# Kernel optimization log

Hardware: AMD Instinct MI355X
Metric: run time of the kernel (lower is better)

Reference implementation:

```python
import jax, jax.numpy as jnp
import numpy as np
from jax import lax

WIN = 7  # hard-coded winsize in PSF.forward
EPS = 1e-8


def _box_sum(x, n):
    # Sliding n x n window sum with zero padding (== ZeroPad2d(n//2) + unfold sum),
    return lax.reduce_window(x, 0.0, lax.add, (1, 1, n, n), (1, 1, 1, 1), 'SAME')


def _patch_stats(x, n):
    n2 = n * n
    s = _box_sum(x, n)
    s2 = _box_sum(x * x, n)
    mean = s / n2
    # torch .var() default is unbiased (divide by N-1)
    var = (s2 - n2 * mean * mean) / (n2 - 1)
    return mean, jnp.maximum(var, 0.0)


def patch_mv_norm(x, n):
    mean, var = _patch_stats(x, n)
    return (x - mean) / (jnp.sqrt(var) + EPS)


def patch_adain(x, y, n):
    x_norm = patch_mv_norm(x, n)
    y_mean, y_var = _patch_stats(y, n)
    return x_norm * jnp.sqrt(y_var) + y_mean  # note: no eps on y_std, as in source


def conv1x1(x, w, b):
    # x: (B,C,H,W), w: (O,C), b: (O,)
    return jnp.einsum('oc,bchw->bohw', w, x) + b[None, :, None, None]


def setup_inputs() -> dict:
    key = jax.random.key(0)
    ks = jax.random.split(key, 12)
    B, C, H, W = 8, 256, 128, 128
    front = jax.random.normal(ks[0], (B, C, H, W), dtype=jnp.float32)
    back = jax.random.normal(ks[1], (B, C, H, W), dtype=jnp.float32)
    mask = jax.random.uniform(ks[2], (B, 1, H, W), dtype=jnp.float32)
    scale = 0.02
    we = jax.random.normal(ks[3], (C, C), dtype=jnp.float32) * scale
    wf = jax.random.normal(ks[4], (C, C), dtype=jnp.float32) * scale
    wg = jax.random.normal(ks[5], (C, C), dtype=jnp.float32) * scale
    wh = jax.random.normal(ks[6], (C, C), dtype=jnp.float32) * scale
    be = jax.random.normal(ks[7], (C,), dtype=jnp.float32) * scale
    bf = jax.random.normal(ks[8], (C,), dtype=jnp.float32) * scale
    bg = jax.random.normal(ks[9], (C,), dtype=jnp.float32) * scale
    bh = jax.random.normal(ks[10], (C,), dtype=jnp.float32) * scale
    return {'front': front, 'back': back, 'mask': mask,
            'we': we, 'be': be, 'wf': wf, 'bf': bf,
            'wg': wg, 'bg': bg, 'wh': wh, 'bh': bh}


def reference(front, back, mask, we, be, wf, bf, wg, bg, wh, bh):
    b, c, h, w = front.shape
    EE = conv1x1(patch_adain(front, back, WIN), we, be)
    FF = conv1x1(patch_mv_norm(front, WIN), wf, bf)
    GG = conv1x1(patch_mv_norm(back, WIN), wg, bg)
    HH = conv1x1(back, wh, bh)
    # channel-wise cosine similarity between FF and GG
    F_n = jnp.sqrt(jnp.sum(FF * FF, axis=1))  # (B,H,W)
    G_n = jnp.sqrt(jnp.sum(GG * GG, axis=1))
    S = jnp.sum(FF * GG, axis=1) / (F_n * G_n)
    # per-sample spatial min-max normalization
    S_flat = S.reshape(b, h * w)
    s_min = jnp.min(S_flat, axis=1, keepdims=True)
    s_max = jnp.max(S_flat, axis=1, keepdims=True)
    S_n = ((S_flat - s_min) / (s_max - s_min)).reshape(b, 1, h, w)
    fused = S_n * EE + (1.0 - S_n) * HH
    return fused
```

## Files before the change

### kernel.cpp

```cpp
#include <hip/hip_runtime.h>
#include <math.h>

#define PIX 16384
#define TSZ ((size_t)33554432)

typedef __attribute__((ext_vector_type(8))) short  short8;
typedef __attribute__((ext_vector_type(4))) float  float4v;
typedef __attribute__((ext_vector_type(4))) unsigned int uint4v;
typedef __attribute__((ext_vector_type(2))) unsigned int uint2v;

__device__ __forceinline__ unsigned short f2bf(float x) {
  unsigned int u = __float_as_uint(x);
  u += 0x7fffu + ((u >> 16) & 1u);
  return (unsigned short)(u >> 16);
}
__device__ __forceinline__ float bf2f(unsigned short h) {
  return __uint_as_float(((unsigned int)h) << 16);
}
__device__ __forceinline__ unsigned int pack_bf2(float lo, float hi) {
  unsigned int ul = __float_as_uint(lo); ul += 0x7fffu + ((ul >> 16) & 1u);
  unsigned int uh = __float_as_uint(hi); uh += 0x7fffu + ((uh >> 16) & 1u);
  return __builtin_amdgcn_perm(uh, ul, 0x07060302u);
}

#define SB0   __builtin_amdgcn_sched_barrier(0)
#define BARR  __builtin_amdgcn_s_barrier()
#define LGKM0 asm volatile("s_waitcnt lgkmcnt(0)" ::: "memory")
#define VMC(n) asm volatile("s_waitcnt vmcnt(" #n ")" ::: "memory")

__global__ __launch_bounds__(256) void k_prep(const float* __restrict__ we,
                                              const float* __restrict__ wf,
                                              const float* __restrict__ wg,
                                              const float* __restrict__ wh,
                                              unsigned short* __restrict__ wbf) {
  int idx = blockIdx.x * 256 + threadIdx.x;
  int g = idx >> 16, within = idx & 65535;
  const float* src = (g == 0) ? wf : (g == 1) ? wg : (g == 2) ? we : wh;
  int e    = within & 7;
  int lane = (within >> 3) & 63;
  int im   = (within >> 9) & 3;
  int wv   = (within >> 11) & 3;
  int i    = within >> 13;
  int col = lane & 15, q = lane >> 4;
  int m = wv * 64 + im * 16 + col;
  int k = i * 32 + q * 8 + e;
  wbf[idx] = f2bf(src[m * 256 + k]);
}

__global__ __launch_bounds__(256, 4) void k_stats(const float* __restrict__ front,
                                                  const float* __restrict__ back,
                                                  unsigned short* __restrict__ xcm) {
  int blk = blockIdx.x;
  int s   = blk & 7;
  int c   = (blk >> 3) & 255;
  int b   = blk >> 11;
  int t   = threadIdx.x;
  int r0  = s * 16;

  __shared__ float2 vspD[16 * 137];

  size_t planeOff = ((size_t)(b * 256 + c)) * PIX;

  float meanR[8], sdR[8];

  #pragma unroll 1
  for (int phase = 0; phase < 2; ++phase) {
    const float* src = (phase == 0 ? back : front) + planeOff;
    {
      int col = t & 127;
      int rg  = (t >> 7) * 8;
      const float* colp = src + col;
      float xv[14];
      #pragma unroll
      for (int j = 0; j < 14; ++j) {
        int g = r0 + rg - 3 + j;
        float v = 0.f;
        if (g >= 0 && g < 128) v = colp[g * 128];
        xv[j] = v;
      }
      float sm = 0.f, s2 = 0.f;
      #pragma unroll
      for (int j = 0; j < 7; ++j) { sm += xv[j]; s2 = fmaf(xv[j], xv[j], s2); }
      vspD[rg * 137 + col + 3] = make_float2(sm, s2);
      #pragma unroll
      for (int o = 1; o < 8; ++o) {
        float vn = xv[o + 6], vo = xv[o - 1];
        sm += vn - vo;
        s2 += vn * vn - vo * vo;
        vspD[(rg + o) * 137 + col + 3] = make_float2(sm, s2);
      }
      if (t < 96) {
        int rr = t & 15;
        int pc = t >> 4;
        int ac = (pc < 3) ? pc : 128 + pc;
        vspD[rr * 137 + ac] = make_float2(0.f, 0.f);
      }
    }
    LGKM0; BARR;
    {
      int r  = t & 15;
      int c0 = (t >> 4) * 8;
      float2 w[14];
      #pragma unroll
      for (int i = 0; i < 14; ++i) w[i] = vspD[r * 137 + c0 + i];
      float4v x0 = *(const float4v*)(src + (r0 + r) * 128 + c0);
      float4v x1 = *(const float4v*)(src + (r0 + r) * 128 + c0 + 4);
      float xc[8] = {x0[0], x0[1], x0[2], x0[3], x1[0], x1[1], x1[2], x1[3]};
      float sm = 0.f, s2 = 0.f;
      #pragma unroll
      for (int i = 0; i < 7; ++i) { sm += w[i].x; s2 += w[i].y; }
      float nrmv[8], hv[8];
      #pragma unroll
      for (int o = 0; o < 8; ++o) {
        float mean = sm * (1.f / 49.f);
        float var  = (s2 - sm * mean) * (1.f / 48.f);
        var = var > 0.f ? var : 0.f;
        float sd = __builtin_amdgcn_sqrtf(var);
        float x  = xc[o];
        float nrm = (x - mean) * __builtin_amdgcn_rcpf(sd + 1e-8f);
        if (phase == 0) { meanR[o] = mean; sdR[o] = sd; hv[o] = x; }
        else            { hv[o] = nrm * sdR[o] + meanR[o]; }
        nrmv[o] = nrm;
        if (o < 7) { sm += w[o + 7].x - w[o].x; s2 += w[o + 7].y - w[o].y; }
      }
      uint4v nv  = (uint4v){pack_bf2(nrmv[0], nrmv[1]), pack_bf2(nrmv[2], nrmv[3]),
                            pack_bf2(nrmv[4], nrmv[5]), pack_bf2(nrmv[6], nrmv[7])};
      uint4v hvv = (uint4v){pack_bf2(hv[0], hv[1]), pack_bf2(hv[2], hv[3]),
                            pack_bf2(hv[4], hv[5]), pack_bf2(hv[6], hv[7])};
      int p = (r0 + r) * 128 + c0;
      size_t gb2 = (((size_t)(b * 256 + (p >> 6))) * 256 + c) * 64 + (p & 63);
      int tn0 = (phase == 0) ? 1 : 0;
      int tn1 = (phase == 0) ? 3 : 2;
      *(uint4v*)(xcm + (size_t)tn0 * TSZ + gb2) = nv;
      *(uint4v*)(xcm + (size_t)tn1 * TSZ + gb2) = hvv;
    }
    LGKM0; BARR;
  }
}

__device__ __forceinline__ void stage_tile(const unsigned short* __restrict__ Xt,
                                           int k0, int t,
                                           unsigned short* dst) {
  int kk = ((t >> 5) << 2) + ((t & 7) >> 1);
  int px = (((t >> 3) & 3) << 4) + ((t & 1) << 3);
  const unsigned short* src = Xt + (size_t)(k0 << 6) + (kk << 6) + px;
  typedef const __attribute__((address_space(1))) unsigned int GUI;
  typedef __attribute__((address_space(3))) unsigned int LUI;
  __builtin_amdgcn_global_load_lds((GUI*)(unsigned long long)src,
                                   (LUI*)(unsigned)(unsigned long long)(dst + t * 8),
                                   16, 0, 0);
}

#define LOADA(S, I) {                                           \
  af[S][0] = *(const short8*)(Wr + (I) * 8192 + 0 * 512);       \
  af[S][1] = *(const short8*)(Wr + (I) * 8192 + 1 * 512);       \
  af[S][2] = *(const short8*)(Wr + (I) * 8192 + 2 * 512);       \
  af[S][3] = *(const short8*)(Wr + (I) * 8192 + 3 * 512); }

#define TR8(O0,O1,O2,O3,O4,O5,O6,O7)                                              \
  asm volatile("ds_read_b64_tr_b16 %0, %1 offset:" #O0 : "=v"(r0) : "v"(tra));    \
  asm volatile("ds_read_b64_tr_b16 %0, %1 offset:" #O1 : "=v"(r1) : "v"(tra));    \
  asm volatile("ds_read_b64_tr_b16 %0, %1 offset:" #O2 : "=v"(r2) : "v"(tra));    \
  asm volatile("ds_read_b64_tr_b16 %0, %1 offset:" #O3 : "=v"(r3) : "v"(tra));    \
  asm volatile("ds_read_b64_tr_b16 %0, %1 offset:" #O4 : "=v"(r4) : "v"(tra));    \
  asm volatile("ds_read_b64_tr_b16 %0, %1 offset:" #O5 : "=v"(r5) : "v"(tra));    \
  asm volatile("ds_read_b64_tr_b16 %0, %1 offset:" #O6 : "=v"(r6) : "v"(tra));    \
  asm volatile("ds_read_b64_tr_b16 %0, %1 offset:" #O7 : "=v"(r7) : "v"(tra));

#define DOMFMA(MS) {                                                        \
  union BU { unsigned u[4]; short8 s; } bu0, bu1, bu2, bu3;                 \
  bu0.u[0]=r0[0]; bu0.u[1]=r0[1]; bu0.u[2]=r1[0]; bu0.u[3]=r1[1];           \
  bu1.u[0]=r2[0]; bu1.u[1]=r2[1]; bu1.u[2]=r3[0]; bu1.u[3]=r3[1];           \
  bu2.u[0]=r4[0]; bu2.u[1]=r4[1]; bu2.u[2]=r5[0]; bu2.u[3]=r5[1];           \
  bu3.u[0]=r6[0]; bu3.u[1]=r6[1]; bu3.u[2]=r7[0]; bu3.u[3]=r7[1];           \
  short8 bv0 = bu0.s, bv1 = bu1.s, bv2 = bu2.s, bv3 = bu3.s;                \
  _Pragma("unroll")                                                         \
  for (int im = 0; im < 4; ++im) {                                          \
    acc[0][im] = __builtin_amdgcn_mfma_f32_16x16x32_bf16(af[MS][im], bv0, acc[0][im], 0, 0, 0); \
    acc[1][im] = __builtin_amdgcn_mfma_f32_16x16x32_bf16(af[MS][im], bv1, acc[1][im], 0, 0, 0); \
    acc[2][im] = __builtin_amdgcn_mfma_f32_16x16x32_bf16(af[MS][im], bv2, acc[2][im], 0, 0, 0); \
    acc[3][im] = __builtin_amdgcn_mfma_f32_16x16x32_bf16(af[MS][im], bv3, acc[3][im], 0, 0, 0); \
  } }

#define GSTEP(VN, DOSTAGE, K0, SLOT, DOA, AS, AI, MS, O0,O1,O2,O3,O4,O5,O6,O7) \
  SB0;                                                                          \
  if (DOSTAGE) stage_tile(X, K0, t, xt + (SLOT) * 2048);                        \
  SB0;                                                                          \
  if (DOA) LOADA(AS, AI);                                                       \
  SB0;                                                                          \
  VMC(VN);                                                                      \
  SB0; BARR; SB0;                                                               \
  TR8(O0,O1,O2,O3,O4,O5,O6,O7);                                                 \
  LGKM0; SB0;                                                                   \
  DOMFMA(MS);

__device__ __forceinline__ void gemm_pipe(const unsigned short* __restrict__ X,
                                          const unsigned short* __restrict__ Wm,
                                          unsigned short* xt, unsigned xbase,
                                          int mbase, int lane, int t,
                                          float4v acc[4][4]) {
  unsigned tra = xbase + (unsigned)((((lane >> 4)) << 10) + ((lane & 15) << 3));
  const unsigned short* __restrict__ Wr = Wm + ((mbase >> 6) << 11) + lane * 8;

  short8 af[3][4];
  uint2v r0, r1, r2, r3, r4, r5, r6, r7;

  #pragma unroll
  for (int in = 0; in < 4; ++in)
    #pragma unroll
    for (int im = 0; im < 4; ++im)
      acc[in][im] = (float4v){0.f, 0.f, 0.f, 0.f};

  SB0; BARR; SB0;
  stage_tile(X,  0, t, xt + 0 * 2048);
  stage_tile(X, 32, t, xt + 1 * 2048);
  stage_tile(X, 64, t, xt + 2 * 2048);
  SB0;
  LOADA(0, 0);
  SB0;
  LOADA(1, 1);
  SB0;

  GSTEP( 9,  1,  96,  3,   1, 2, 2, 0,      0,  512,  128,  640,  256,  768,  384,  896)
  GSTEP(10,  1, 128,  4,   1, 0, 3, 1,   4096, 4608, 4224, 4736, 4352, 4864, 4480, 4992)
  GSTEP(10,  1, 160,  0,   1, 1, 4, 2,   8192, 8704, 8320, 8832, 8448, 8960, 8576, 9088)
  GSTEP(10,  1, 192,  1,   1, 2, 5, 0,  12288,12800,12416,12928,12544,13056,12672,13184)
  GSTEP(10,  1, 224,  2,   1, 0, 6, 1,  16384,16896,16512,17024,16640,17152,16768,17280)
  GSTEP( 9,  0,   0,  0,   1, 1, 7, 2,      0,  512,  128,  640,  256,  768,  384,  896)
  GSTEP( 4,  0,   0,  0,   0, 0, 0, 0,   4096, 4608, 4224, 4736, 4352, 4864, 4480, 4992)
  GSTEP( 0,  0,   0,  0,   0, 0, 0, 1,   8192, 8704, 8320, 8832, 8448, 8960, 8576, 9088)
}

__global__ __launch_bounds__(256, 2) void k_gemm1(const unsigned short* __restrict__ xcm,
                                                  const unsigned short* __restrict__ wbf,
                                                  const float* __restrict__ bFF,
                                                  const float* __restrict__ bGG,
                                                  float* __restrict__ Sout) {
  int blk  = blockIdx.x;
  int b    = blk >> 8;
  int pt   = blk & 255;
  int p0   = pt * 64;
  int t    = threadIdx.x;
  int wv   = t >> 6;
  int lane = t & 63;
  int q    = lane >> 4;
  int mbase = wv * 64;

  __shared__ __align__(16) unsigned short xt[5][2048];
  __shared__ float sred[3 * 64];
  if (t < 192) sred[t] = 0.f;
  __syncthreads();
  unsigned xbase = (unsigned)(unsigned long long)&xt[0][0];

  const unsigned short* Xt = xcm + (((size_t)(b * 256 + pt)) << 14);

  float4v aF[4][4], aG[4][4];

  gemm_pipe(Xt + 0 * TSZ, wbf + 0 * 65536, &xt[0][0], xbase, mbase, lane, t, aF);
  gemm_pipe(Xt + 1 * TSZ, wbf + 1 * 65536, &xt[0][0], xbase, mbase, lane, t, aG);
  #pragma unroll
  for (int im = 0; im < 4; ++im) {
    float4v bvF = *(const float4v*)(bFF + mbase + im * 16 + q * 4);
    float4v bvG = *(const float4v*)(bGG + mbase + im * 16 + q * 4);
    #pragma unroll
    for (int in = 0; in < 4; ++in) { aF[in][im] += bvF; aG[in][im] += bvG; }
  }
  #pragma unroll
  for (int in = 0; in < 4; ++in) {
    float d = 0.f, nf = 0.f, ng = 0.f;
    #pragma unroll
    for (int im = 0; im < 4; ++im)
      #pragma unroll
      for (int r = 0; r < 4; ++r) {
        float f = aF[in][im][r], g = aG[in][im][r];
        d += f * g; nf += f * f; ng += g * g;
      }
    d  += __shfl_xor(d, 16);  d  += __shfl_xor(d, 32);
    nf += __shfl_xor(nf, 16); nf += __shfl_xor(nf, 32);
    ng += __shfl_xor(ng, 16); ng += __shfl_xor(ng, 32);
    if (lane < 16) {
      atomicAdd(&sred[0 * 64 + in * 16 + lane], d);
      atomicAdd(&sred[1 * 64 + in * 16 + lane], nf);
      atomicAdd(&sred[2 * 64 + in * 16 + lane], ng);
    }
  }
  __syncthreads();
  if (t < 64) {
    float d = sred[t], nf = sred[64 + t], ng = sred[128 + t];
    Sout[(size_t)b * PIX + p0 + t] = d / (sqrtf(nf) * sqrtf(ng));
  }
}

__global__ __launch_bounds__(256, 2) void k_gemm2(const unsigned short* __restrict__ xcm,
                                                  const unsigned short* __restrict__ wbf,
                                                  const float* __restrict__ bEE,
                                                  const float* __restrict__ bHH,
                                                  const float* __restrict__ S,
                                                  const float* __restrict__ mm,
                                                  float* __restrict__ out) {
  int blk  = blockIdx.x;
  int b    = blk >> 8;
  int pt   = blk & 255;
  int p0   = pt * 64;
  int t    = threadIdx.x;
  int wv   = t >> 6;
  int lane = t & 63;
  int col  = lane & 15;
  int q    = lane >> 4;
  int mbase = wv * 64;

  __shared__ __align__(16) unsigned short xt[5][2048];
  unsigned xbase = (unsigned)(unsigned long long)&xt[0][0];

  const unsigned short* Xt = xcm + (((size_t)(b * 256 + pt)) << 14);

  float4v aE[4][4], aH[4][4];

  gemm_pipe(Xt + 2 * TSZ, wbf + 2 * 65536, &xt[0][0], xbase, mbase, lane, t, aE);
  gemm_pipe(Xt + 3 * TSZ, wbf + 3 * 65536, &xt[0][0], xbase, mbase, lane, t, aH);

  float mn = mm[b * 2], mx = mm[b * 2 + 1];
  float inv = 1.f / (mx - mn);
  float sn[4];
  #pragma unroll
  for (int in = 0; in < 4; ++in)
    sn[in] = (S[(size_t)b * PIX + p0 + in * 16 + col] - mn) * inv;

  #pragma unroll
  for (int im = 0; im < 4; ++im) {
    float4v bvE = *(const float4v*)(bEE + mbase + im * 16 + q * 4);
    float4v bvH = *(const float4v*)(bHH + mbase + im * 16 + q * 4);
    #pragma unroll
    for (int in = 0; in < 4; ++in)
      #pragma unroll
      for (int r = 0; r < 4; ++r) {
        int m = mbase + im * 16 + q * 4 + r;
        float e = aE[in][im][r] + bvE[r];
        float h = aH[in][im][r] + bvH[r];
        out[((size_t)(b * 256 + m)) * PIX + p0 + in * 16 + col] = h + sn[in] * (e - h);
      }
  }
}

__global__ __launch_bounds__(256) void k_minmax(const float* __restrict__ S,
                                                float* __restrict__ mm) {
  int b = blockIdx.x, t = threadIdx.x;
  const float* sp = S + (size_t)b * PIX;
  float mn = 3.0e38f, mx = -3.0e38f;
  for (int i = t; i < PIX; i += 256) { float v = sp[i]; mn = fminf(mn, v); mx = fmaxf(mx, v); }
  #pragma unroll
  for (int o = 32; o >= 1; o >>= 1) {
    mn = fminf(mn, __shfl_xor(mn, o));
    mx = fmaxf(mx, __shfl_xor(mx, o));
  }
  __shared__ float smn[4], smx[4];
  if ((t & 63) == 0) { smn[t >> 6] = mn; smx[t >> 6] = mx; }
  __syncthreads();
  if (t == 0) {
    mn = fminf(fminf(smn[0], smn[1]), fminf(smn[2], smn[3]));
    mx = fmaxf(fmaxf(smx[0], smx[1]), fmaxf(smx[2], smx[3]));
    mm[b * 2] = mn; mm[b * 2 + 1] = mx;
  }
}

extern "C" void kernel_launch(void* const* d_in, const int* in_sizes, int n_in,
                              void* d_out, int out_size, void* d_ws, size_t ws_size,
                              hipStream_t stream) {
  const float* front = (const float*)d_in[0];
  const float* back  = (const float*)d_in[1];
  const float* we = (const float*)d_in[3];
  const float* be = (const float*)d_in[4];
  const float* wf = (const float*)d_in[5];
  const float* bf = (const float*)d_in[6];
  const float* wg = (const float*)d_in[7];
  const float* bg = (const float*)d_in[8];
  const float* wh = (const float*)d_in[9];
  const float* bh = (const float*)d_in[10];

  char* ws = (char*)d_ws;
  unsigned short* xcm  = (unsigned short*)(ws);
  unsigned short* wbf  = (unsigned short*)(ws + 268435456);
  float*          S    = (float*)(ws + 268959744);
  float*          mm   = (float*)(ws + 269484032);
  float*          out  = (float*)d_out;

  k_prep  <<<1024,  256, 0, stream>>>(we, wf, wg, wh, wbf);
  k_stats <<<16384, 256, 0, stream>>>(front, back, xcm);
  k_gemm1 <<<2048,  256, 0, stream>>>(xcm, wbf, bf, bg, S);
  k_minmax<<<8,     256, 0, stream>>>(S, mm);
  k_gemm2 <<<2048,  256, 0, stream>>>(xcm, wbf, be, bh, S, mm, out);
}
```

Baseline: 512.0 us.

## Stage all K tiles in LDS and cut per-step barriers in gemm pipeline

The GEMM pipeline used a 5-slot rotating LDS ring with one barrier per 32-wide K step. It now enlarges LDS to 8 slots so the whole K=256 panel is resident, and processes two K steps per barrier. That halves the barrier count and drops the slot reuse that forced waits. The cost is more LDS per block (32KB vs 20KB), which could limit occupancy, and coarser waits on the vector-memory counter.

```diff
diff --git a/kernel.cpp b/kernel.cpp
--- a/kernel.cpp
+++ b/kernel.cpp
@@ -182,18 +182,6 @@
     acc[3][im] = __builtin_amdgcn_mfma_f32_16x16x32_bf16(af[MS][im], bv3, acc[3][im], 0, 0, 0); \
   } }
 
-#define GSTEP(VN, DOSTAGE, K0, SLOT, DOA, AS, AI, MS, O0,O1,O2,O3,O4,O5,O6,O7) \
-  SB0;                                                                          \
-  if (DOSTAGE) stage_tile(X, K0, t, xt + (SLOT) * 2048);                        \
-  SB0;                                                                          \
-  if (DOA) LOADA(AS, AI);                                                       \
-  SB0;                                                                          \
-  VMC(VN);                                                                      \
-  SB0; BARR; SB0;                                                               \
-  TR8(O0,O1,O2,O3,O4,O5,O6,O7);                                                 \
-  LGKM0; SB0;                                                                   \
-  DOMFMA(MS);
-
 __device__ __forceinline__ void gemm_pipe(const unsigned short* __restrict__ X,
                                           const unsigned short* __restrict__ Wm,
                                           unsigned short* xt, unsigned xbase,
@@ -202,7 +190,7 @@
   unsigned tra = xbase + (unsigned)((((lane >> 4)) << 10) + ((lane & 15) << 3));
   const unsigned short* __restrict__ Wr = Wm + ((mbase >> 6) << 11) + lane * 8;
 
-  short8 af[3][4];
+  short8 af[2][4];
   uint2v r0, r1, r2, r3, r4, r5, r6, r7;
 
   #pragma unroll
@@ -212,23 +200,44 @@
       acc[in][im] = (float4v){0.f, 0.f, 0.f, 0.f};
 
   SB0; BARR; SB0;
-  stage_tile(X,  0, t, xt + 0 * 2048);
-  stage_tile(X, 32, t, xt + 1 * 2048);
-  stage_tile(X, 64, t, xt + 2 * 2048);
-  SB0;
-  LOADA(0, 0);
-  SB0;
-  LOADA(1, 1);
-  SB0;
-
-  GSTEP( 9,  1,  96,  3,   1, 2, 2, 0,      0,  512,  128,  640,  256,  768,  384,  896)
-  GSTEP(10,  1, 128,  4,   1, 0, 3, 1,   4096, 4608, 4224, 4736, 4352, 4864, 4480, 4992)
-  GSTEP(10,  1, 160,  0,   1, 1, 4, 2,   8192, 8704, 8320, 8832, 8448, 8960, 8576, 9088)
-  GSTEP(10,  1, 192,  1,   1, 2, 5, 0,  12288,12800,12416,12928,12544,13056,12672,13184)
-  GSTEP(10,  1, 224,  2,   1, 0, 6, 1,  16384,16896,16512,17024,16640,17152,16768,17280)
-  GSTEP( 9,  0,   0,  0,   1, 1, 7, 2,      0,  512,  128,  640,  256,  768,  384,  896)
-  GSTEP( 4,  0,   0,  0,   0, 0, 0, 0,   4096, 4608, 4224, 4736, 4352, 4864, 4480, 4992)
-  GSTEP( 0,  0,   0,  0,   0, 0, 0, 1,   8192, 8704, 8320, 8832, 8448, 8960, 8576, 9088)
+  stage_tile(X,   0, t, xt + 0 * 2048);
+  stage_tile(X,  32, t, xt + 1 * 2048);
+  stage_tile(X,  64, t, xt + 2 * 2048);
+  stage_tile(X,  96, t, xt + 3 * 2048);
+  SB0;
+
+  LOADA(0, 0); LOADA(1, 1);
+  SB0;
+  stage_tile(X, 128, t, xt + 4 * 2048);
+  stage_tile(X, 160, t, xt + 5 * 2048);
+  SB0;
+  VMC(2); SB0; BARR; SB0;
+  TR8(    0,   512,   128,   640,   256,   768,   384,   896); LGKM0; SB0; DOMFMA(0);
+  TR8( 4096,  4608,  4224,  4736,  4352,  4864,  4480,  4992); LGKM0; SB0; DOMFMA(1);
+
+  SB0;
+  LOADA(0, 2); LOADA(1, 3);
+  SB0;
+  stage_tile(X, 192, t, xt + 6 * 2048);
+  stage_tile(X, 224, t, xt + 7 * 2048);
+  SB0;
+  VMC(2); SB0; BARR; SB0;
+  TR8( 8192,  8704,  8320,  8832,  8448,  8960,  8576,  9088); LGKM0; SB0; DOMFMA(0);
+  TR8(12288, 12800, 12416, 12928, 12544, 13056, 12672, 13184); LGKM0; SB0; DOMFMA(1);
+
+  SB0;
+  LOADA(0, 4); LOADA(1, 5);
+  SB0;
+  VMC(0); SB0; BARR; SB0;
+  TR8(16384, 16896, 16512, 17024, 16640, 17152, 16768, 17280); LGKM0; SB0; DOMFMA(0);
+  TR8(20480, 20992, 20608, 21120, 20736, 21248, 20864, 21376); LGKM0; SB0; DOMFMA(1);
+
+  SB0;
+  LOADA(0, 6); LOADA(1, 7);
+  SB0;
+  VMC(0); SB0; BARR; SB0;
+  TR8(24576, 25088, 24704, 25216, 24832, 25344, 24960, 25472); LGKM0; SB0; DOMFMA(0);
+  TR8(28672, 29184, 28800, 29312, 28928, 29440, 29056, 29568); LGKM0; SB0; DOMFMA(1);
 }
 
 __global__ __launch_bounds__(256, 2) void k_gemm1(const unsigned short* __restrict__ xcm,
@@ -246,7 +255,7 @@
   int q    = lane >> 4;
   int mbase = wv * 64;
 
-  __shared__ __align__(16) unsigned short xt[5][2048];
+  __shared__ __align__(16) unsigned short xt[8][2048];
   __shared__ float sred[3 * 64];
   if (t < 192) sred[t] = 0.f;
   __syncthreads();
@@ -309,7 +318,7 @@
   int q    = lane >> 4;
   int mbase = wv * 64;
 
-  __shared__ __align__(16) unsigned short xt[5][2048];
+  __shared__ __align__(16) unsigned short xt[8][2048];
   unsigned xbase = (unsigned)(unsigned long long)&xt[0][0];
 
   const unsigned short* Xt = xcm + (((size_t)(b * 256 + pt)) << 14);
```

After: 511.5 us. Within noise of the previous version (-0.1%).
